# Performance work log

Measured on AMD Instinct MI355X. Metric: run time of the kernel, lower is better.

## Reference

```python
import jax, jax.numpy as jnp
import numpy as np

WIDTH = 64
MODES = 64
NBLOCKS = 4
PAD = 2
DT = 1.0
FSTRENGTH = 2.0
FORDER = 8


def _phi1(z, eps=1e-6):
    small = jnp.abs(z) < eps
    series = 1.0 + z * 0.5 + z * z / 6.0
    safe = (jnp.exp(z) - 1.0) / jnp.where(small, 1.0, z)
    return jnp.where(small, series, safe)


def _smooth_filter(m, strength, order):
    g = jnp.linspace(0.0, 1.0, m)
    r = jnp.sqrt(g * g + 1e-12)
    return jnp.exp(-strength * r ** order)


def setup_inputs() -> dict:
    key = jax.random.key(0)
    ks = jax.random.split(key, 12)
    B, X, IS, NC = 16, 16384, 10, 3
    W, M, NB = WIDTH, MODES, NBLOCKS
    H = 2 * W
    inp = {}
    inp["x"] = jax.random.normal(ks[0], (B, X, IS * NC), jnp.float32)
    inp["grid"] = jax.random.uniform(ks[1], (B, X, 1), jnp.float32)
    def lin(k, o, i):
        return jax.random.normal(k, (o, i), jnp.float32) / np.sqrt(i).astype(np.float32)
    inp["fc0_w"] = lin(ks[2], W, IS * NC + 1); inp["fc0_b"] = jnp.zeros((W,), jnp.float32)
    inp["fc1_w"] = lin(ks[3], 128, W); inp["fc1_b"] = jnp.zeros((128,), jnp.float32)
    inp["fc2_w"] = lin(ks[4], NC, 128); inp["fc2_b"] = jnp.zeros((NC,), jnp.float32)
    inp["g_w1"] = jax.random.normal(ks[5], (NB, H, W), jnp.float32) / np.sqrt(W).astype(np.float32)
    inp["g_b1"] = jnp.zeros((NB, H), jnp.float32)
    inp["g_w2"] = jax.random.normal(ks[6], (NB, W, H), jnp.float32) / np.sqrt(H).astype(np.float32)
    inp["g_b2"] = jnp.zeros((NB, W), jnp.float32)
    inp["w_w"] = jax.random.normal(ks[7], (NB, W, W), jnp.float32) / np.sqrt(W).astype(np.float32)
    inp["w_b"] = jnp.zeros((NB, W), jnp.float32)
    inp["log_decay"] = jax.random.normal(ks[8], (NB, W, M), jnp.float32) * 0.1
    scale = 1.0 / (W * W)
    inp["mix_re"] = scale * jax.random.uniform(ks[9], (NB, W, W, M), jnp.float32)
    inp["mix_im"] = scale * jax.random.uniform(ks[10], (NB, W, W, M), jnp.float32)
    inp["alpha_w_raw"] = jnp.asarray(np.log(np.expm1(0.6)), jnp.float32)
    inp["alpha_g_raw"] = jnp.asarray(np.log(np.expm1(1.0)), jnp.float32)
    return inp


def reference(x, grid, fc0_w, fc0_b, fc1_w, fc1_b, fc2_w, fc2_b,
              g_w1, g_b1, g_w2, g_b2, w_w, w_b, log_decay, mix_re, mix_im,
              alpha_w_raw, alpha_g_raw):
    gelu = lambda t: jax.nn.gelu(t, approximate=False)  # torch default GELU is exact erf
    # lift: cat grid, fc0, move channels first, pad right
    h = jnp.concatenate([x, grid], axis=-1) @ fc0_w.T + fc0_b      # [B,X,W]
    h = jnp.transpose(h, (0, 2, 1))                                 # [B,W,X]
    h = jnp.pad(h, ((0, 0), (0, 0), (0, PAD)))                      # [B,W,Xp]
    Xp = h.shape[-1]
    aw = jax.nn.softplus(alpha_w_raw)
    ag = jax.nn.softplus(alpha_g_raw)
    filt = _smooth_filter(MODES, FSTRENGTH, FORDER)                 # [M]
    for i in range(NBLOCKS):
        # pointwise MLP g(x) (1x1 convs == channel matmuls)
        gmid = gelu(jnp.einsum('oc,bcx->box', g_w1[i], h) + g_b1[i][None, :, None])
        g = ag * (jnp.einsum('oc,bcx->box', g_w2[i], gmid) + g_b2[i][None, :, None])
        # spectral ETD step
        v_hat = jnp.fft.rfft(h)                                     # [B,W,Xp//2+1] complex
        g_hat = jnp.fft.rfft(g)
        lam = -jax.nn.softplus(log_decay[i])                        # [W,M], beta=0 so real
        z = DT * lam
        expz = jnp.exp(z)[None]                                     # [1,W,M]
        phi = _phi1(z)[None]
        mix = mix_re[i] + 1j * mix_im[i]                            # [W,W,M]
        gm = jnp.einsum('bim,iom->bom', g_hat[:, :, :MODES], mix)
        out_m = expz * v_hat[:, :, :MODES] + (DT * phi * gm) * filt[None, None, :]
        out_hat = jnp.concatenate([out_m, jnp.zeros_like(v_hat[:, :, MODES:])], axis=-1)
        etd_out = jnp.fft.irfft(out_hat, n=Xp)
        # skip path: 1x1 conv, scaled (inner_steps=1 -> w_scale=1)
        wout = jnp.einsum('oc,bcx->box', w_w[i], h) + w_b[i][None, :, None]
        upd = etd_out + aw * wout
        h = upd if i == NBLOCKS - 1 else gelu(upd)
    h = h[..., :-PAD]
    h = jnp.transpose(h, (0, 2, 1))                                 # [B,X,W]
    h = gelu(h @ fc1_w.T + fc1_b)
    h = h @ fc2_w.T + fc2_b
    return h[:, :, None, :]                                         # [B,X,1,NC]
```

## Files before the change

kernel.cpp:

```cpp
#include <hip/hip_runtime.h>
#include <hip/hip_bf16.h>


#define BB 16
#define X 16384
#define XP 16386
#define XPAD 16512
#define W 64
#define H 128
#define M 64
#define NB 4
#define NC 3

typedef __hip_bfloat16 bf16;
typedef __attribute__((ext_vector_type(8))) short short8;
typedef __attribute__((ext_vector_type(4))) float floatx4;

__device__ __forceinline__ float gelu_f(float x){
  float x3 = x * x * x;
  float y2 = 1.5957691216f * x + 0.0713548162f * x3;
  float e = __expf(y2);
  float th = 1.f - 2.f / (e + 1.f);
  return 0.5f * x * (1.f + th);
}
__device__ __forceinline__ float softplus_f(float v){
  return (v > 20.f) ? v : log1pf(expf(v));
}
__device__ __forceinline__ short f2bs(float f){
  union { float f; unsigned u; } v; v.f = f;
  unsigned r = (v.u + 0x7FFFu + ((v.u >> 16) & 1u)) >> 16;
  return (short)r;
}
__device__ __forceinline__ float bs2f(short s){
  union { unsigned u; float f; } v; v.u = ((unsigned)(unsigned short)s) << 16;
  return v.f;
}
#define MFMA(a,b,c) __builtin_amdgcn_mfma_f32_16x16x32_bf16((a),(b),(c),0,0,0)

__global__ __launch_bounds__(256) void k_basisT(short* __restrict__ basT16){
  int idx = blockIdx.x * 256 + threadIdx.x;
  if (idx >= 128 * XPAD) return;
  int mp = idx / XPAD, x = idx - mp * XPAD;
  float v = 0.f;
  if (x < XP){
    int m = mp >> 1;
    int tt = (int)(((long long)x * (long long)m) % XP);
    float ang = 6.283185307179586477f * (float)tt / (float)XP;
    float s, c; sincosf(ang, &s, &c);
    v = (mp & 1) ? s : c;
  }
  basT16[idx] = f2bs(v);
}
__global__ __launch_bounds__(256) void k_basisC(short* __restrict__ basC16){
  int idx = blockIdx.x * 256 + threadIdx.x;
  if (idx >= XPAD * 128) return;
  int x = idx >> 7, kp = idx & 127;
  float v = 0.f;
  if (x < XP){
    int m = kp >> 1;
    int tt = (int)(((long long)x * (long long)m) % XP);
    float ang = 6.283185307179586477f * (float)tt / (float)XP;
    float s, c; sincosf(ang, &s, &c);
    v = (kp & 1) ? -s : c;
  }
  basC16[idx] = f2bs(v);
}

__global__ __launch_bounds__(256) void k_decay(const float* __restrict__ log_decay,
                                               float* __restrict__ expz,
                                               float* __restrict__ phi){
  int idx = blockIdx.x * 256 + threadIdx.x;
  if (idx >= NB * W * M) return;
  float z = -softplus_f(log_decay[idx]);
  expz[idx] = expf(z);
  float p;
  if (fabsf(z) < 1e-6f) p = 1.0f + 0.5f * z + z * z * (1.0f / 6.0f);
  else                  p = expm1f(z) / z;
  phi[idx] = p;
}

__global__ void k_filt(float* __restrict__ filt){
  int m = threadIdx.x;
  if (m < M){
    float g = (float)m / 63.0f;
    float r2 = g * g + 1e-12f;
    float r4 = r2 * r2;
    float r8 = r4 * r4;
    filt[m] = expf(-2.0f * r8);
  }
}

__global__ __launch_bounds__(256) void k_prep(const float* __restrict__ w_w,
                                              const float* __restrict__ g_w1,
                                              const float* __restrict__ fc1_w,
                                              const float* __restrict__ fc0_w,
                                              const float* __restrict__ awr,
                                              short* __restrict__ ww16,
                                              short* __restrict__ w116,
                                              short* __restrict__ w1fc16,
                                              short* __restrict__ w0fc16){
  int idx = blockIdx.x * 256 + threadIdx.x;
  float aw = softplus_f(awr[0]);
  if (idx < 16384){ ww16[idx] = f2bs(aw * w_w[idx]); }
  else if (idx < 49152){ int i = idx - 16384; w116[i] = f2bs(g_w1[i]); }
  else if (idx < 57344){ int i = idx - 49152; w1fc16[i] = f2bs(fc1_w[i]); }
  else if (idx < 59392){
    int i = idx - 57344;
    int o = i >> 5, f = i & 31;
    w0fc16[i] = (f < 31) ? f2bs(fc0_w[o * 31 + f]) : (short)0;
  }
}

__global__ __launch_bounds__(256) void k_fc0m(const float* __restrict__ xg,
                                              const float* __restrict__ gg,
                                              const short* __restrict__ w0fc16,
                                              const float* __restrict__ bg,
                                              short* __restrict__ h16,
                                              short* __restrict__ hX){
  __shared__ short xs16[128][40];
  __shared__ short xp[128][72];
  int b = blockIdx.y, bx = blockIdx.x, x0 = bx * 128, t = threadIdx.x;
  if (bx == 128){
    for (int i = t; i < 64 * 128; i += 256){
      int c = i >> 7, x = i & 127;
      h16[((size_t)b * 64 + c) * XPAD + x0 + x] = 0;
    }
    short8 z8 = (short8){0,0,0,0,0,0,0,0};
    for (int u = 0; u < 4; ++u){
      int idx = u * 256 + t;
      int x = idx >> 3, col = (idx & 7) * 8;
      *(short8*)&hX[((size_t)b * XPAD + x0 + x) * 64 + col] = z8;
    }
    return;
  }
  for (int i = t; i < 3840; i += 256){
    int x = i / 30, f = i - x * 30;
    xs16[x][f] = f2bs(xg[((size_t)b * X + x0 + x) * 30 + f]);
  }
  if (t < 128){ xs16[t][30] = f2bs(gg[(size_t)b * X + x0 + t]); xs16[t][31] = 0; }
  __syncthreads();
  int w = t >> 6, l = t & 63, q = l >> 4, ln = l & 15;
  floatx4 acc[4][2];
  #pragma unroll
  for (int mt = 0; mt < 4; ++mt)
    #pragma unroll
    for (int nt = 0; nt < 2; ++nt) acc[mt][nt] = (floatx4){0.f,0.f,0.f,0.f};
  #pragma unroll
  for (int mt = 0; mt < 4; ++mt){
    short8 av = *(const short8*)&w0fc16[(mt * 16 + ln) * 32 + q * 8];
    #pragma unroll
    for (int nt = 0; nt < 2; ++nt){
      short8 bv = *(const short8*)&xs16[w * 32 + nt * 16 + ln][q * 8];
      acc[mt][nt] = MFMA(av, bv, acc[mt][nt]);
    }
  }
  #pragma unroll
  for (int mt = 0; mt < 4; ++mt)
    #pragma unroll
    for (int r = 0; r < 4; ++r){
      int o = mt * 16 + q * 4 + r;
      float bias = bg[o];
      #pragma unroll
      for (int nt = 0; nt < 2; ++nt){
        int xl = w * 32 + nt * 16 + ln;
        short s = f2bs(acc[mt][nt][r] + bias);
        h16[((size_t)b * 64 + o) * XPAD + x0 + xl] = s;
        xp[xl][o] = s;
      }
    }
  __syncthreads();
  #pragma unroll
  for (int u = 0; u < 4; ++u){
    int idx = u * 256 + t;
    int x = idx >> 3, col = (idx & 7) * 8;
    *(short8*)&hX[((size_t)b * XPAD + x0 + x) * 64 + col] = *(const short8*)&xp[x][col];
  }
}

__global__ __launch_bounds__(256) void k_dft(const short* __restrict__ h16,
                                             const short* __restrict__ hX,
                                             const short* __restrict__ w116,
                                             const float* __restrict__ b1g,
                                             const short* __restrict__ basT16,
                                             float* __restrict__ vhat,
                                             float* __restrict__ gmidhat, int blk){
  __shared__ __align__(16) char smem[52224];
  short (*srcT)[136] = (short(*)[136])smem;
  short (*hT)[72]    = (short(*)[72])(smem + 17408);
  short (*basS)[136] = (short(*)[136])(smem + 17408);
  int b = blockIdx.y, z = blockIdx.z, bx = blockIdx.x, t = threadIdx.x;
  int w = t >> 6, l = t & 63, q = l >> 4, ln = l & 15;
  const short* hbase = h16 + (size_t)b * 64 * XPAD;
  const short* hXb   = hX + (size_t)b * XPAD * 64;
  floatx4 acc[8];
  #pragma unroll
  for (int i = 0; i < 8; ++i) acc[i] = (floatx4){0.f,0.f,0.f,0.f};
  short8 aw1[2];
  float bias[4];
  if (z){
    #pragma unroll
    for (int ks = 0; ks < 2; ++ks)
      aw1[ks] = *(const short8*)&w116[((size_t)blk * H + (z-1)*64 + w*16 + ln) * 64 + ks*32 + q*8];
    #pragma unroll
    for (int r = 0; r < 4; ++r)
      bias[r] = b1g[blk * H + (z-1)*64 + w*16 + q*4 + r];
  }
  for (int ci = bx; ci < 129; ci += 16){
    int xc = ci * 128;
    __syncthreads();
    if (z == 0){
      #pragma unroll
      for (int u = 0; u < 4; ++u){
        int idx = u * 256 + t;
        int c = idx >> 4, col = (idx & 15) * 8;
        *(short8*)&srcT[c][col] = *(const short8*)&hbase[(size_t)c * XPAD + xc + col];
      }
    } else {
      #pragma unroll
      for (int u = 0; u < 4; ++u){
        int idx = u * 256 + t;
        int x = idx >> 3, col = (idx & 7) * 8;
        *(short8*)&hT[x][col] = *(const short8*)&hXb[(size_t)(xc + x) * 64 + col];
      }
    }
    __syncthreads();
    if (z){
      floatx4 a2[8];
      #pragma unroll
      for (int i = 0; i < 8; ++i) a2[i] = (floatx4){0.f,0.f,0.f,0.f};
      #pragma unroll
      for (int ks = 0; ks < 2; ++ks){
        #pragma unroll
        for (int nt = 0; nt < 8; ++nt){
          short8 bv = *(const short8*)&hT[nt*16 + ln][ks*32 + q*8];
          a2[nt] = MFMA(aw1[ks], bv, a2[nt]);
        }
      }
      #pragma unroll
      for (int nt = 0; nt < 8; ++nt){
        int gx = xc + nt*16 + ln;
        #pragma unroll
        for (int r = 0; r < 4; ++r){
          int o = w*16 + q*4 + r;
          float vv = gelu_f(a2[nt][r] + bias[r]);
          srcT[o][nt*16 + ln] = (gx < XP) ? f2bs(vv) : (short)0;
        }
      }
    }
    __syncthreads();
    #pragma unroll
    for (int u = 0; u < 8; ++u){
      int idx = u * 256 + t;
      int mp = idx >> 4, col = (idx & 15) * 8;
      *(short8*)&basS[mp][col] = *(const short8*)&basT16[(size_t)mp * XPAD + xc + col];
    }
    __syncthreads();
    #pragma unroll
    for (int ks = 0; ks < 4; ++ks){
      short8 av = *(const short8*)&srcT[w*16 + ln][ks*32 + q*8];
      #pragma unroll
      for (int nt = 0; nt < 8; ++nt){
        short8 bv = *(const short8*)&basS[nt*16 + ln][ks*32 + q*8];
        acc[nt] = MFMA(av, bv, acc[nt]);
      }
    }
  }
  #pragma unroll
  for (int nt = 0; nt < 8; ++nt)
    #pragma unroll
    for (int r = 0; r < 4; ++r){
      int mp = nt*16 + ln;
      int c  = w*16 + q*4 + r;
      float v = acc[nt][r];
      if (mp & 1) v = -v;
      if (z == 0) atomicAdd(&vhat[((size_t)b * W + c) * 128 + mp], v);
      else atomicAdd(&gmidhat[((size_t)b * H + (z-1)*64 + c) * 128 + mp], v);
    }
}

__global__ __launch_bounds__(256) void k_ghat(const float* __restrict__ gmidhat,
                                              const float* __restrict__ w2g,
                                              const float* __restrict__ b2g,
                                              const float* __restrict__ agr,
                                              float* __restrict__ ghat, int blk){
  __shared__ float w2s[64][133];
  int b = blockIdx.x, zg = blockIdx.y, t = threadIdx.x;
  float ag = softplus_f(agr[0]);
  for (int i = t; i < 8192; i += 256) w2s[i >> 7][i & 127] = w2g[(size_t)blk * 8192 + i];
  __syncthreads();
  int i = t & 63, ms = t >> 6;
  int mp0 = zg * 16 + ms * 4;
  for (int j = 0; j < 4; ++j){
    int mp = mp0 + j;
    float acc = 0.f;
    for (int c2 = 0; c2 < H; ++c2)
      acc = fmaf(w2s[i][c2], gmidhat[((size_t)b * H + c2) * 128 + mp], acc);
    if (mp == 0) acc += (float)XP * b2g[blk * W + i];
    ghat[((size_t)b * W + i) * 128 + mp] = ag * acc;
  }
}

__global__ __launch_bounds__(256) void k_outm(const float* __restrict__ vhat,
                       const float* __restrict__ ghat,
                       const float* __restrict__ mix_re, const float* __restrict__ mix_im,
                       const float* __restrict__ expz, const float* __restrict__ phi,
                       const float* __restrict__ filt, short* __restrict__ outm16, int blk){
  int b = blockIdx.y, t = threadIdx.x;
  int m = t & 63, os = t >> 6;
  int o = blockIdx.x * 4 + os;
  const float* mre = mix_re + (size_t)blk * W * W * M + (size_t)o * M + m;
  const float* mim = mix_im + (size_t)blk * W * W * M + (size_t)o * M + m;
  float gr = 0.f, gi = 0.f;
  for (int i = 0; i < W; ++i){
    float gre = ghat[((size_t)b * W + i) * 128 + 2 * m];
    float gim = ghat[((size_t)b * W + i) * 128 + 2 * m + 1];
    float xr = mre[(size_t)i * W * M];
    float xi = mim[(size_t)i * W * M];
    gr = fmaf(gre, xr, gr); gr = fmaf(-gim, xi, gr);
    gi = fmaf(gre, xi, gi); gi = fmaf( gim, xr, gi);
  }
  int om = blk * W * M + o * M + m;
  float ez = expz[om], ph = phi[om], fl = filt[m];
  float vr = vhat[((size_t)b * W + o) * 128 + 2 * m];
  float vi = vhat[((size_t)b * W + o) * 128 + 2 * m + 1];
  float outr = fmaf(ez, vr, ph * fl * gr);
  float outi = fmaf(ez, vi, ph * fl * gi);
  float sc = ((m == 0) ? 1.0f : 2.0f) / (float)XP;
  outm16[((size_t)b * W + o) * 128 + 2 * m]     = f2bs(outr * sc);
  outm16[((size_t)b * W + o) * 128 + 2 * m + 1] = f2bs(outi * sc);
}

__global__ __launch_bounds__(256) void k_update(short* __restrict__ h16,
                                                short* __restrict__ hX,
                                                const short* __restrict__ outm16,
                                                const short* __restrict__ basC16,
                                                const short* __restrict__ ww16,
                                                const float* __restrict__ wbg,
                                                const float* __restrict__ awr, int blk){
  __shared__ __align__(16) char smem[52224];
  short (*hT)[72]    = (short(*)[72])smem;
  short (*wwS)[72]   = (short(*)[72])(smem + 18432);
  short (*basS)[136] = (short(*)[136])smem;
  short (*omS)[136]  = (short(*)[136])(smem + 34816);
  short (*xp)[72]    = (short(*)[72])smem;
  int b = blockIdx.y, x0 = blockIdx.x * 128, t = threadIdx.x;
  int w = t >> 6, l = t & 63, q = l >> 4, ln = l & 15;
  float aw = softplus_f(awr[0]);
  const short* hXb = hX + (size_t)b * XPAD * 64;
  #pragma unroll
  for (int u = 0; u < 4; ++u){
    int idx = u * 256 + t;
    int x = idx >> 3, col = (idx & 7) * 8;
    *(short8*)&hT[x][col] = *(const short8*)&hXb[(size_t)(x0 + x) * 64 + col];
  }
  #pragma unroll
  for (int u = 0; u < 2; ++u){
    int idx = u * 256 + t;
    int o = idx >> 3, col = (idx & 7) * 8;
    *(short8*)&wwS[o][col] = *(const short8*)&ww16[((size_t)blk * W + o) * 64 + col];
  }
  __syncthreads();
  floatx4 acc[2][4];
  #pragma unroll
  for (int mt = 0; mt < 2; ++mt)
    #pragma unroll
    for (int nt = 0; nt < 4; ++nt) acc[mt][nt] = (floatx4){0.f,0.f,0.f,0.f};
  #pragma unroll
  for (int ks = 0; ks < 2; ++ks){
    short8 a0 = *(const short8*)&hT[(w*2+0)*16 + ln][ks*32 + q*8];
    short8 a1 = *(const short8*)&hT[(w*2+1)*16 + ln][ks*32 + q*8];
    #pragma unroll
    for (int nt = 0; nt < 4; ++nt){
      short8 bv = *(const short8*)&wwS[nt*16 + ln][ks*32 + q*8];
      acc[0][nt] = MFMA(a0, bv, acc[0][nt]);
      acc[1][nt] = MFMA(a1, bv, acc[1][nt]);
    }
  }
  __syncthreads();
  #pragma unroll
  for (int u = 0; u < 8; ++u){
    int idx = u * 256 + t;
    int x = idx >> 4, col = (idx & 15) * 8;
    *(short8*)&basS[x][col] = *(const short8*)&basC16[(size_t)(x0 + x) * 128 + col];
  }
  #pragma unroll
  for (int u = 0; u < 4; ++u){
    int idx = u * 256 + t;
    int o = idx >> 4, col = (idx & 15) * 8;
    *(short8*)&omS[o][col] = *(const short8*)&outm16[((size_t)b * W + o) * 128 + col];
  }
  __syncthreads();
  #pragma unroll
  for (int ks = 0; ks < 4; ++ks){
    short8 a0 = *(const short8*)&basS[(w*2+0)*16 + ln][ks*32 + q*8];
    short8 a1 = *(const short8*)&basS[(w*2+1)*16 + ln][ks*32 + q*8];
    #pragma unroll
    for (int nt = 0; nt < 4; ++nt){
      short8 bv = *(const short8*)&omS[nt*16 + ln][ks*32 + q*8];
      acc[0][nt] = MFMA(a0, bv, acc[0][nt]);
      acc[1][nt] = MFMA(a1, bv, acc[1][nt]);
    }
  }
  short sreg[2][4][4];
  #pragma unroll
  for (int mt = 0; mt < 2; ++mt)
    #pragma unroll
    for (int nt = 0; nt < 4; ++nt){
      int o = nt*16 + ln;
      int xbase = x0 + (w*2+mt)*16 + q*4;
      float wbv = aw * wbg[blk * W + o];
      short* hp = &h16[((size_t)b * 64 + o) * XPAD + xbase];
      #pragma unroll
      for (int r = 0; r < 4; ++r){
        float u = acc[mt][nt][r] + wbv;
        if (blk != NB - 1) u = gelu_f(u);
        sreg[mt][nt][r] = f2bs(u);
      }
      if (xbase + 3 < XP){
        *(short4*)hp = *(short4*)&sreg[mt][nt][0];
      } else {
        #pragma unroll
        for (int r = 0; r < 4; ++r)
          if (xbase + r < XP) hp[r] = sreg[mt][nt][r];
      }
    }
  __syncthreads();
  #pragma unroll
  for (int mt = 0; mt < 2; ++mt)
    #pragma unroll
    for (int nt = 0; nt < 4; ++nt){
      int o = nt*16 + ln;
      int xl = (w*2+mt)*16 + q*4;
      #pragma unroll
      for (int r = 0; r < 4; ++r) xp[xl + r][o] = sreg[mt][nt][r];
    }
  __syncthreads();
  #pragma unroll
  for (int u = 0; u < 4; ++u){
    int idx = u * 256 + t;
    int x = idx >> 3, col = (idx & 7) * 8;
    if (x0 + x < XP)
      *(short8*)&hX[((size_t)b * XPAD + x0 + x) * 64 + col] = *(const short8*)&xp[x][col];
  }
}

__global__ __launch_bounds__(256) void k_fc12(const short* __restrict__ hX,
                                              const short* __restrict__ w1fc16,
                                              const float* __restrict__ b1,
                                              const float* __restrict__ w2,
                                              const float* __restrict__ b2,
                                              float* __restrict__ out){
  __shared__ short hT[128][72];
  __shared__ short gT[128][136];
  __shared__ float w2s[NC][132];
  __shared__ float red[2][128][NC];
  int b = blockIdx.y, x0 = blockIdx.x * 128, t = threadIdx.x;
  int w = t >> 6, l = t & 63, q = l >> 4, ln = l & 15;
  const short* hXb = hX + (size_t)b * XPAD * 64;
  #pragma unroll
  for (int u = 0; u < 4; ++u){
    int idx = u * 256 + t;
    int x = idx >> 3, col = (idx & 7) * 8;
    *(short8*)&hT[x][col] = *(const short8*)&hXb[(size_t)(x0 + x) * 64 + col];
  }
  for (int i = t; i < NC * H; i += 256) w2s[i / H][i % H] = w2[i];
  __syncthreads();
  floatx4 acc[2][8];
  #pragma unroll
  for (int mt = 0; mt < 2; ++mt)
    #pragma unroll
    for (int nt = 0; nt < 8; ++nt) acc[mt][nt] = (floatx4){0.f,0.f,0.f,0.f};
  #pragma unroll
  for (int ks = 0; ks < 2; ++ks){
    short8 a0 = *(const short8*)&w1fc16[(size_t)((w*2+0)*16 + ln) * 64 + ks*32 + q*8];
    short8 a1 = *(const short8*)&w1fc16[(size_t)((w*2+1)*16 + ln) * 64 + ks*32 + q*8];
    #pragma unroll
    for (int nt = 0; nt < 8; ++nt){
      short8 bv = *(const short8*)&hT[nt*16 + ln][ks*32 + q*8];
      acc[0][nt] = MFMA(a0, bv, acc[0][nt]);
      acc[1][nt] = MFMA(a1, bv, acc[1][nt]);
    }
  }
  #pragma unroll
  for (int mt = 0; mt < 2; ++mt){
    float bvv[4];
    #pragma unroll
    for (int r = 0; r < 4; ++r) bvv[r] = b1[(w*2+mt)*16 + q*4 + r];
    #pragma unroll
    for (int nt = 0; nt < 8; ++nt){
      int x = nt*16 + ln;
      #pragma unroll
      for (int r = 0; r < 4; ++r)
        gT[x][(w*2+mt)*16 + q*4 + r] = f2bs(gelu_f(acc[mt][nt][r] + bvv[r]));
    }
  }
  __syncthreads();
  int x = t & 127, half = t >> 7;
  float a3[NC] = {0.f, 0.f, 0.f};
  for (int og = 0; og < 8; ++og){
    int o0 = half * 64 + og * 8;
    short8 gv = *(const short8*)&gT[x][o0];
    #pragma unroll
    for (int j = 0; j < 8; ++j){
      float gf = bs2f(gv[j]);
      #pragma unroll
      for (int n = 0; n < NC; ++n) a3[n] = fmaf(gf, w2s[n][o0 + j], a3[n]);
    }
  }
  #pragma unroll
  for (int n = 0; n < NC; ++n) red[half][x][n] = a3[n];
  __syncthreads();
  if (half == 0){
    #pragma unroll
    for (int n = 0; n < NC; ++n)
      out[((size_t)b * X + x0 + x) * NC + n] = red[0][x][n] + red[1][x][n] + b2[n];
  }
}

extern "C" void kernel_launch(void* const* d_in, const int* in_sizes, int n_in,
                              void* d_out, int out_size, void* d_ws, size_t ws_size,
                              hipStream_t stream){
  (void)in_sizes; (void)n_in; (void)out_size; (void)ws_size;
  const float* x        = (const float*)d_in[0];
  const float* grid     = (const float*)d_in[1];
  const float* fc0_w    = (const float*)d_in[2];
  const float* fc0_b    = (const float*)d_in[3];
  const float* fc1_w    = (const float*)d_in[4];
  const float* fc1_b    = (const float*)d_in[5];
  const float* fc2_w    = (const float*)d_in[6];
  const float* fc2_b    = (const float*)d_in[7];
  const float* g_w1     = (const float*)d_in[8];
  const float* g_b1     = (const float*)d_in[9];
  const float* g_w2     = (const float*)d_in[10];
  const float* g_b2     = (const float*)d_in[11];
  const float* w_w      = (const float*)d_in[12];
  const float* w_b      = (const float*)d_in[13];
  const float* log_dec  = (const float*)d_in[14];
  const float* mix_re   = (const float*)d_in[15];
  const float* mix_im   = (const float*)d_in[16];
  const float* a_w      = (const float*)d_in[17];
  const float* a_g      = (const float*)d_in[18];
  float* out = (float*)d_out;

  short* basC16 = (short*)d_ws;
  short* basT16 = basC16 + (size_t)XPAD * 128;
  short* h16    = basT16 + (size_t)128 * XPAD;
  short* hX     = h16 + (size_t)BB * 64 * XPAD;
  float* vhat   = (float*)(hX + (size_t)BB * XPAD * 64);
  float* gmidhat= vhat + (size_t)BB * W * 128;
  float* ghat   = gmidhat + (size_t)BB * H * 128;
  float* expz   = ghat + (size_t)BB * W * 128;
  float* phi    = expz + NB * W * M;
  float* filt   = phi + NB * W * M;
  short* outm16 = (short*)(filt + 64);
  short* ww16   = outm16 + (size_t)BB * W * 128;
  short* w116   = ww16 + NB * W * W;
  short* w1fc16 = w116 + NB * H * W;
  short* w0fc16 = w1fc16 + H * W;

  k_basisT<<<dim3((128 * XPAD + 255) / 256), 256, 0, stream>>>(basT16);
  k_basisC<<<dim3((XPAD * 128 + 255) / 256), 256, 0, stream>>>(basC16);
  k_decay<<<dim3((NB * W * M + 255) / 256), 256, 0, stream>>>(log_dec, expz, phi);
  k_filt<<<1, 64, 0, stream>>>(filt);
  k_prep<<<dim3(232), 256, 0, stream>>>(w_w, g_w1, fc1_w, fc0_w, a_w, ww16, w116, w1fc16, w0fc16);
  k_fc0m<<<dim3(129, BB), 256, 0, stream>>>(x, grid, w0fc16, fc0_b, h16, hX);

  for (int blk = 0; blk < NB; ++blk){
    hipMemsetAsync(vhat, 0, (size_t)(BB * W * 128 + BB * H * 128) * sizeof(float), stream);
    k_dft<<<dim3(16, BB, 3), 256, 0, stream>>>(h16, hX, w116, g_b1, basT16, vhat, gmidhat, blk);
    k_ghat<<<dim3(BB, 8), 256, 0, stream>>>(gmidhat, g_w2, g_b2, a_g, ghat, blk);
    k_outm<<<dim3(16, BB), 256, 0, stream>>>(vhat, ghat, mix_re, mix_im, expz, phi, filt, outm16, blk);
    k_update<<<dim3(XPAD / 128, BB), 256, 0, stream>>>(h16, hX, outm16, basC16, ww16, w_b, a_w, blk);
  }
  k_fc12<<<dim3(X / 128, BB), 256, 0, stream>>>(hX, w1fc16, fc1_b, fc2_w, fc2_b, out);
}
```

Baseline: 633.6 us.

## Rebalance DFT work split and halve update-kernel shared memory

The DFT kernel now uses a flat 48-block grid and assigns 10 blocks to the cheap z=0 path and 19 each to the two GELU-heavy paths. This is meant to balance per-block work, and the LDS row pitch is padded from 136 to 140 to reduce bank conflicts. The update kernel splits its K=128 inverse-DFT matmul into two halves that reuse one 64-wide basis buffer, cutting LDS from 52KB to 36KB so more blocks can be resident per CU. In exchange it adds an extra sync and a second basis load phase.

```diff
diff --git a/kernel.cpp b/kernel.cpp
--- a/kernel.cpp
+++ b/kernel.cpp
@@ -184,11 +184,15 @@
                                              const short* __restrict__ basT16,
                                              float* __restrict__ vhat,
                                              float* __restrict__ gmidhat, int blk){
-  __shared__ __align__(16) char smem[52224];
-  short (*srcT)[136] = (short(*)[136])smem;
-  short (*hT)[72]    = (short(*)[72])(smem + 17408);
-  short (*basS)[136] = (short(*)[136])(smem + 17408);
-  int b = blockIdx.y, z = blockIdx.z, bx = blockIdx.x, t = threadIdx.x;
+  __shared__ __align__(16) char smem[53760];
+  short (*srcT)[140] = (short(*)[140])smem;
+  short (*hT)[72]    = (short(*)[72])(smem + 17920);
+  short (*basS)[140] = (short(*)[140])(smem + 17920);
+  int b = blockIdx.y, k = blockIdx.x, t = threadIdx.x;
+  int z, base, nwg;
+  if (k < 10){ z = 0; base = k; nwg = 10; }
+  else if (k < 29){ z = 1; base = k - 10; nwg = 19; }
+  else { z = 2; base = k - 29; nwg = 19; }
   int w = t >> 6, l = t & 63, q = l >> 4, ln = l & 15;
   const short* hbase = h16 + (size_t)b * 64 * XPAD;
   const short* hXb   = hX + (size_t)b * XPAD * 64;
@@ -205,7 +209,7 @@
     for (int r = 0; r < 4; ++r)
       bias[r] = b1g[blk * H + (z-1)*64 + w*16 + q*4 + r];
   }
-  for (int ci = bx; ci < 129; ci += 16){
+  for (int ci = base; ci < 129; ci += nwg){
     int xc = ci * 128;
     __syncthreads();
     if (z == 0){
@@ -337,13 +341,14 @@
                                                 const short* __restrict__ ww16,
                                                 const float* __restrict__ wbg,
                                                 const float* __restrict__ awr, int blk){
-  __shared__ __align__(16) char smem[52224];
-  short (*hT)[72]    = (short(*)[72])smem;
-  short (*wwS)[72]   = (short(*)[72])(smem + 18432);
-  short (*basS)[136] = (short(*)[136])smem;
-  short (*omS)[136]  = (short(*)[136])(smem + 34816);
-  short (*xp)[72]    = (short(*)[72])smem;
-  int b = blockIdx.y, x0 = blockIdx.x * 128, t = threadIdx.x;
+  __shared__ __align__(16) char smem[36864];
+  short (*hT)[72]   = (short(*)[72])smem;
+  short (*basH)[72] = (short(*)[72])smem;
+  short (*xp)[72]   = (short(*)[72])smem;
+  short (*wwS)[72]  = (short(*)[72])(smem + 18432);
+  short (*omH0)[72] = (short(*)[72])(smem + 18432);
+  short (*omH1)[72] = (short(*)[72])(smem + 27648);
+  int b = blockIdx.y, ci = blockIdx.x, x0 = ci * 128, t = threadIdx.x;
   int w = t >> 6, l = t & 63, q = l >> 4, ln = l & 15;
   float aw = softplus_f(awr[0]);
   const short* hXb = hX + (size_t)b * XPAD * 64;
@@ -378,25 +383,45 @@
   }
   __syncthreads();
   #pragma unroll
-  for (int u = 0; u < 8; ++u){
-    int idx = u * 256 + t;
-    int x = idx >> 4, col = (idx & 15) * 8;
-    *(short8*)&basS[x][col] = *(const short8*)&basC16[(size_t)(x0 + x) * 128 + col];
-  }
-  #pragma unroll
   for (int u = 0; u < 4; ++u){
     int idx = u * 256 + t;
-    int o = idx >> 4, col = (idx & 15) * 8;
-    *(short8*)&omS[o][col] = *(const short8*)&outm16[((size_t)b * W + o) * 128 + col];
-  }
-  __syncthreads();
-  #pragma unroll
-  for (int ks = 0; ks < 4; ++ks){
-    short8 a0 = *(const short8*)&basS[(w*2+0)*16 + ln][ks*32 + q*8];
-    short8 a1 = *(const short8*)&basS[(w*2+1)*16 + ln][ks*32 + q*8];
+    int x = idx >> 3, col = (idx & 7) * 8;
+    *(short8*)&basH[x][col] = *(const short8*)&basC16[(size_t)(x0 + x) * 128 + col];
+  }
+  #pragma unroll
+  for (int u = 0; u < 2; ++u){
+    int idx = u * 256 + t;
+    int o = idx >> 3, col = (idx & 7) * 8;
+    *(short8*)&omH0[o][col] = *(const short8*)&outm16[((size_t)b * W + o) * 128 + col];
+    *(short8*)&omH1[o][col] = *(const short8*)&outm16[((size_t)b * W + o) * 128 + 64 + col];
+  }
+  __syncthreads();
+  #pragma unroll
+  for (int ks = 0; ks < 2; ++ks){
+    short8 a0 = *(const short8*)&basH[(w*2+0)*16 + ln][ks*32 + q*8];
+    short8 a1 = *(const short8*)&basH[(w*2+1)*16 + ln][ks*32 + q*8];
     #pragma unroll
     for (int nt = 0; nt < 4; ++nt){
-      short8 bv = *(const short8*)&omS[nt*16 + ln][ks*32 + q*8];
+      short8 bv = *(const short8*)&omH0[nt*16 + ln][ks*32 + q*8];
+      acc[0][nt] = MFMA(a0, bv, acc[0][nt]);
+      acc[1][nt] = MFMA(a1, bv, acc[1][nt]);
+    }
+  }
+  __syncthreads();
+  #pragma unroll
+  for (int u = 0; u < 4; ++u){
+    int idx = u * 256 + t;
+    int x = idx >> 3, col = (idx & 7) * 8;
+    *(short8*)&basH[x][col] = *(const short8*)&basC16[(size_t)(x0 + x) * 128 + 64 + col];
+  }
+  __syncthreads();
+  #pragma unroll
+  for (int ks = 0; ks < 2; ++ks){
+    short8 a0 = *(const short8*)&basH[(w*2+0)*16 + ln][ks*32 + q*8];
+    short8 a1 = *(const short8*)&basH[(w*2+1)*16 + ln][ks*32 + q*8];
+    #pragma unroll
+    for (int nt = 0; nt < 4; ++nt){
+      short8 bv = *(const short8*)&omH1[nt*16 + ln][ks*32 + q*8];
       acc[0][nt] = MFMA(a0, bv, acc[0][nt]);
       acc[1][nt] = MFMA(a1, bv, acc[1][nt]);
     }
@@ -567,7 +592,7 @@
 
   for (int blk = 0; blk < NB; ++blk){
     hipMemsetAsync(vhat, 0, (size_t)(BB * W * 128 + BB * H * 128) * sizeof(float), stream);
-    k_dft<<<dim3(16, BB, 3), 256, 0, stream>>>(h16, hX, w116, g_b1, basT16, vhat, gmidhat, blk);
+    k_dft<<<dim3(48, BB), 256, 0, stream>>>(h16, hX, w116, g_b1, basT16, vhat, gmidhat, blk);
     k_ghat<<<dim3(BB, 8), 256, 0, stream>>>(gmidhat, g_w2, g_b2, a_g, ghat, blk);
     k_outm<<<dim3(16, BB), 256, 0, stream>>>(vhat, ghat, mix_re, mix_im, expz, phi, filt, outm16, blk);
     k_update<<<dim3(XPAD / 128, BB), 256, 0, stream>>>(h16, hX, outm16, basC16, ww16, w_b, a_w, blk);
```

After: 975.8 us. +54.0%, slower.
